# Performance work log

Measured on AMD Instinct MI355X. Metric: run time of the kernel, lower is better.

## Reference

```python
import jax, jax.numpy as jnp
import numpy as np
import math

PROJ_EPS = 0.001
C_CURV = 0.5  # hyperbolic curvature c


def setup_inputs() -> dict:
    key = jax.random.key(0)
    k1, k2, k3 = jax.random.split(key, 3)
    B, C, H, W, N = 4, 256, 256, 256, 19
    x = jax.random.normal(k1, (B, C, H, W), dtype=jnp.float32)
    # kaiming_uniform_(a=sqrt(5)) on (N, C): bound = sqrt(6 / ((1+5) * fan_in)) = 1/sqrt(C)
    bound = 1.0 / math.sqrt(C)
    P_MLR = jax.random.uniform(k2, (N, C), jnp.float32, -bound, bound)
    A_MLR = jax.random.uniform(k3, (N, C), jnp.float32, -bound, bound)
    return {"x": x, "P_MLR": P_MLR, "A_MLR": A_MLR}


def reference(x, P_MLR, A_MLR):
    K = jnp.float32(C_CURV)
    eps = jnp.float32(1e-12)

    xx = jnp.sum(x * x, axis=1)                       # (B,H,W)  ||x||^2
    pp = jnp.sum(P_MLR * P_MLR, axis=1)               # (N,)     ||-P||^2
    # 1x1 conv with kernel -P: channel contraction
    px = jnp.einsum('bchw,nc->bnhw', x, -P_MLR)       # (B,N,H,W)

    xx_b = xx[:, None]                                # (B,1,H,W)
    pp_b = pp[None, :, None, None]                    # (1,N,1,1)

    sqsq = (K * xx_b) * (K * pp_b)
    A = 1.0 + 2.0 * K * px + K * xx_b
    Bc = 1.0 - K * pp_b
    D = 1.0 + 2.0 * K * px + sqsq
    D = jnp.maximum(D, eps)
    alpha = A / D
    beta = Bc / D

    mobaddnorm = alpha * alpha * pp_b + beta * beta * xx_b + 2.0 * alpha * beta * px
    maxnorm = (1.0 - PROJ_EPS) / jnp.sqrt(K)
    sqrtm = jnp.sqrt(mobaddnorm)
    project_normalized = jnp.where(sqrtm > maxnorm,
                                   maxnorm / jnp.maximum(sqrtm, eps),
                                   jnp.ones_like(mobaddnorm))
    mobaddnormprojected = jnp.where(sqrtm < maxnorm, mobaddnorm,
                                    jnp.full_like(mobaddnorm, maxnorm * maxnorm))

    A_norm = jnp.linalg.norm(A_MLR, axis=1)           # (N,)
    normed_A = A_MLR / jnp.maximum(A_norm, eps)[:, None]  # torch F.normalize (eps=1e-12)

    xdota = beta * jnp.einsum('bchw,nc->bnhw', x, normed_A)
    pdota = alpha * jnp.sum(-P_MLR * normed_A, axis=1)[None, :, None, None]
    mobdota = (xdota + pdota) * project_normalized

    lamb_px = 2.0 / jnp.maximum(1.0 - K * mobaddnormprojected, eps)
    sineterm = jnp.sqrt(K) * mobdota * lamb_px
    out = (2.0 / jnp.sqrt(K)) * A_norm[None, :, None, None] * jnp.arcsinh(sineterm)
    return out
```

## Files before the change

### kernel.cpp

```cpp
#include <hip/hip_runtime.h>
#include <math.h>

#define C_DIM 256
#define N_DIM 19
#define HW 65536
#define CQ 64
#define PP_OFF (N_DIM * C_DIM)
#define PA_OFF (PP_OFF + 32)
#define AN_OFF (PP_OFF + 64)

__global__ void prep_kernel(const float* __restrict__ P,
                            const float* __restrict__ A,
                            float* __restrict__ ws) {
    int n = blockIdx.x;
    int lane = threadIdx.x;
    float pp = 0.f, aa = 0.f, pa = 0.f;
    for (int c = lane; c < C_DIM; c += 64) {
        float p = P[n * C_DIM + c];
        float a = A[n * C_DIM + c];
        pp += p * p;
        aa += a * a;
        pa += p * a;
    }
#pragma unroll
    for (int off = 32; off > 0; off >>= 1) {
        pp += __shfl_xor(pp, off);
        aa += __shfl_xor(aa, off);
        pa += __shfl_xor(pa, off);
    }
    float an  = sqrtf(aa);
    float inv = 1.0f / fmaxf(an, 1e-12f);
    for (int c = lane; c < C_DIM; c += 64) {
        ws[n * C_DIM + c] = A[n * C_DIM + c] * inv;
    }
    if (lane == 0) {
        ws[PP_OFF + n] = pp;
        ws[PA_OFF + n] = -pa * inv;
        ws[AN_OFF + n] = an;
    }
}

__global__ __launch_bounds__(256, 4) void hyper_mlr_main(
    const float* __restrict__ x, const float* __restrict__ P,
    const float* __restrict__ ws, float* __restrict__ out)
{
    __shared__ float4 sP4[N_DIM * CQ];
    __shared__ float4 sA4[N_DIM * CQ];
    __shared__ float  spp[N_DIM], spa[N_DIM], san[N_DIM];

    const float4* P4 = reinterpret_cast<const float4*>(P);
    const float4* W4 = reinterpret_cast<const float4*>(ws);
    for (int i = threadIdx.x; i < N_DIM * CQ; i += 256) {
        float4 pv = P4[i];
        sP4[i] = make_float4(-pv.x, -pv.y, -pv.z, -pv.w);
        sA4[i] = W4[i];
    }
    if (threadIdx.x < N_DIM) {
        spp[threadIdx.x] = ws[PP_OFF + threadIdx.x];
        spa[threadIdx.x] = ws[PA_OFF + threadIdx.x];
        san[threadIdx.x] = ws[AN_OFF + threadIdx.x];
    }
    __syncthreads();

    int tid = blockIdx.x * 256 + threadIdx.x;
    int b   = tid >> 16;
    int hw  = tid & 65535;
    const float* xb = x + (size_t)b * C_DIM * HW + hw;

    float xx = 0.f;
    float px[N_DIM], xa[N_DIM];
#pragma unroll
    for (int n = 0; n < N_DIM; ++n) { px[n] = 0.f; xa[n] = 0.f; }

    float x0 = xb[0];
    float x1 = xb[(size_t)HW];
    float x2 = xb[(size_t)2 * HW];
    float x3 = xb[(size_t)3 * HW];

#pragma unroll 2
    for (int cq = 0; cq < CQ - 1; ++cq) {
        const float* xn = xb + (size_t)(cq + 1) * 4 * HW;
        float n0 = xn[0];
        float n1 = xn[(size_t)HW];
        float n2 = xn[(size_t)2 * HW];
        float n3 = xn[(size_t)3 * HW];

        xx += x0 * x0; xx += x1 * x1; xx += x2 * x2; xx += x3 * x3;
#pragma unroll
        for (int n = 0; n < N_DIM; ++n) {
            float4 p = sP4[n * CQ + cq];
            float4 a = sA4[n * CQ + cq];
            px[n] += x0 * p.x; px[n] += x1 * p.y; px[n] += x2 * p.z; px[n] += x3 * p.w;
            xa[n] += x0 * a.x; xa[n] += x1 * a.y; xa[n] += x2 * a.z; xa[n] += x3 * a.w;
        }
        x0 = n0; x1 = n1; x2 = n2; x3 = n3;
    }
    {
        const int cq = CQ - 1;
        xx += x0 * x0; xx += x1 * x1; xx += x2 * x2; xx += x3 * x3;
#pragma unroll
        for (int n = 0; n < N_DIM; ++n) {
            float4 p = sP4[n * CQ + cq];
            float4 a = sA4[n * CQ + cq];
            px[n] += x0 * p.x; px[n] += x1 * p.y; px[n] += x2 * p.z; px[n] += x3 * p.w;
            xa[n] += x0 * a.x; xa[n] += x1 * a.y; xa[n] += x2 * a.z; xa[n] += x3 * a.w;
        }
    }

    const float K        = 0.5f;
    const float sqK      = 0.70710678118654752f;
    const float maxnorm  = 0.999f / sqK;
    const float maxnorm2 = maxnorm * maxnorm;
    const float eps      = 1e-12f;

    float* ob = out + (size_t)b * N_DIM * HW + hw;
#pragma unroll
    for (int n = 0; n < N_DIM; ++n) {
        float pp = spp[n];
        float pa = spa[n];
        float an = san[n];
        float pxs = px[n], xas = xa[n];

        float Av = 1.0f + pxs + K * xx;
        float Bv = 1.0f - K * pp;
        float D  = fmaxf(1.0f + pxs + (K * K) * xx * pp, eps);
        float alpha = Av / D, beta = Bv / D;
        float mob = alpha * alpha * pp + beta * beta * xx + 2.0f * alpha * beta * pxs;
        float sqrtm = sqrtf(fmaxf(mob, 0.0f));
        float proj = (sqrtm > maxnorm) ? (maxnorm / fmaxf(sqrtm, eps)) : 1.0f;
        float mobp = (sqrtm < maxnorm) ? mob : maxnorm2;
        float mobdota = (beta * xas + alpha * pa) * proj;
        float lamb = 2.0f / fmaxf(1.0f - K * mobp, eps);
        float sine = sqK * mobdota * lamb;
        ob[(size_t)n * HW] = (2.0f / sqK) * an * asinhf(sine);
    }
}

extern "C" void kernel_launch(void* const* d_in, const int* in_sizes, int n_in,
                              void* d_out, int out_size, void* d_ws, size_t ws_size,
                              hipStream_t stream) {
    const float* x  = (const float*)d_in[0];
    const float* P  = (const float*)d_in[1];
    const float* A  = (const float*)d_in[2];
    float* out = (float*)d_out;
    float* ws  = (float*)d_ws;

    prep_kernel<<<N_DIM, 64, 0, stream>>>(P, A, ws);
    hyper_mlr_main<<<1024, 256, 0, stream>>>(x, P, ws, out);
}
```

Measured before the change: 434.6 us.

## Read weights via uniform scalar loads from interleaved global table instead of LDS

The prep kernel now writes an interleaved table, ordered by channel-quad then class, holding negated P and normalized A. The main kernel drops its shared-memory staging and __syncthreads and reads the weights straight from global memory with wave-uniform addresses, which the compiler can turn into scalar (SMEM) loads, removing LDS traffic from the inner loop. It also drops the occupancy hint in launch_bounds and the unroll-2 pragma. The risk is scalar-cache latency and SGPR pressure in the inner loop, and possibly lower occupancy.

```diff
diff --git a/kernel.cpp b/kernel.cpp
--- a/kernel.cpp
+++ b/kernel.cpp
@@ -5,23 +5,21 @@
 #define N_DIM 19
 #define HW 65536
 #define CQ 64
-#define PP_OFF (N_DIM * C_DIM)
-#define PA_OFF (PP_OFF + 32)
-#define AN_OFF (PP_OFF + 64)
+#define TBL (CQ * N_DIM * 8)
+#define PP_OFF TBL
+#define PA_OFF (TBL + 32)
+#define AN_OFF (TBL + 64)
 
 __global__ void prep_kernel(const float* __restrict__ P,
                             const float* __restrict__ A,
                             float* __restrict__ ws) {
     int n = blockIdx.x;
     int lane = threadIdx.x;
-    float pp = 0.f, aa = 0.f, pa = 0.f;
-    for (int c = lane; c < C_DIM; c += 64) {
-        float p = P[n * C_DIM + c];
-        float a = A[n * C_DIM + c];
-        pp += p * p;
-        aa += a * a;
-        pa += p * a;
-    }
+    float4 pv = *reinterpret_cast<const float4*>(P + n * C_DIM + lane * 4);
+    float4 av = *reinterpret_cast<const float4*>(A + n * C_DIM + lane * 4);
+    float pp = pv.x * pv.x + pv.y * pv.y + pv.z * pv.z + pv.w * pv.w;
+    float aa = av.x * av.x + av.y * av.y + av.z * av.z + av.w * av.w;
+    float pa = pv.x * av.x + pv.y * av.y + pv.z * av.z + pv.w * av.w;
 #pragma unroll
     for (int off = 32; off > 0; off >>= 1) {
         pp += __shfl_xor(pp, off);
@@ -30,9 +28,11 @@
     }
     float an  = sqrtf(aa);
     float inv = 1.0f / fmaxf(an, 1e-12f);
-    for (int c = lane; c < C_DIM; c += 64) {
-        ws[n * C_DIM + c] = A[n * C_DIM + c] * inv;
-    }
+
+    float* o = ws + (size_t)(lane * N_DIM + n) * 8;
+    o[0] = -pv.x; o[1] = -pv.y; o[2] = -pv.z; o[3] = -pv.w;
+    o[4] = av.x * inv; o[5] = av.y * inv; o[6] = av.z * inv; o[7] = av.w * inv;
+
     if (lane == 0) {
         ws[PP_OFF + n] = pp;
         ws[PA_OFF + n] = -pa * inv;
@@ -40,28 +40,10 @@
     }
 }
 
-__global__ __launch_bounds__(256, 4) void hyper_mlr_main(
-    const float* __restrict__ x, const float* __restrict__ P,
-    const float* __restrict__ ws, float* __restrict__ out)
+__global__ __launch_bounds__(256) void hyper_mlr_main(
+    const float* __restrict__ x, const float* __restrict__ ws,
+    float* __restrict__ out)
 {
-    __shared__ float4 sP4[N_DIM * CQ];
-    __shared__ float4 sA4[N_DIM * CQ];
-    __shared__ float  spp[N_DIM], spa[N_DIM], san[N_DIM];
-
-    const float4* P4 = reinterpret_cast<const float4*>(P);
-    const float4* W4 = reinterpret_cast<const float4*>(ws);
-    for (int i = threadIdx.x; i < N_DIM * CQ; i += 256) {
-        float4 pv = P4[i];
-        sP4[i] = make_float4(-pv.x, -pv.y, -pv.z, -pv.w);
-        sA4[i] = W4[i];
-    }
-    if (threadIdx.x < N_DIM) {
-        spp[threadIdx.x] = ws[PP_OFF + threadIdx.x];
-        spa[threadIdx.x] = ws[PA_OFF + threadIdx.x];
-        san[threadIdx.x] = ws[AN_OFF + threadIdx.x];
-    }
-    __syncthreads();
-
     int tid = blockIdx.x * 256 + threadIdx.x;
     int b   = tid >> 16;
     int hw  = tid & 65535;
@@ -77,7 +59,6 @@
     float x2 = xb[(size_t)2 * HW];
     float x3 = xb[(size_t)3 * HW];
 
-#pragma unroll 2
     for (int cq = 0; cq < CQ - 1; ++cq) {
         const float* xn = xb + (size_t)(cq + 1) * 4 * HW;
         float n0 = xn[0];
@@ -86,10 +67,11 @@
         float n3 = xn[(size_t)3 * HW];
 
         xx += x0 * x0; xx += x1 * x1; xx += x2 * x2; xx += x3 * x3;
+        const float* wq = ws + (size_t)cq * N_DIM * 8;
 #pragma unroll
         for (int n = 0; n < N_DIM; ++n) {
-            float4 p = sP4[n * CQ + cq];
-            float4 a = sA4[n * CQ + cq];
+            float4 p = *reinterpret_cast<const float4*>(wq + n * 8);
+            float4 a = *reinterpret_cast<const float4*>(wq + n * 8 + 4);
             px[n] += x0 * p.x; px[n] += x1 * p.y; px[n] += x2 * p.z; px[n] += x3 * p.w;
             xa[n] += x0 * a.x; xa[n] += x1 * a.y; xa[n] += x2 * a.z; xa[n] += x3 * a.w;
         }
@@ -98,10 +80,11 @@
     {
         const int cq = CQ - 1;
         xx += x0 * x0; xx += x1 * x1; xx += x2 * x2; xx += x3 * x3;
+        const float* wq = ws + (size_t)cq * N_DIM * 8;
 #pragma unroll
         for (int n = 0; n < N_DIM; ++n) {
-            float4 p = sP4[n * CQ + cq];
-            float4 a = sA4[n * CQ + cq];
+            float4 p = *reinterpret_cast<const float4*>(wq + n * 8);
+            float4 a = *reinterpret_cast<const float4*>(wq + n * 8 + 4);
             px[n] += x0 * p.x; px[n] += x1 * p.y; px[n] += x2 * p.z; px[n] += x3 * p.w;
             xa[n] += x0 * a.x; xa[n] += x1 * a.y; xa[n] += x2 * a.z; xa[n] += x3 * a.w;
         }
@@ -116,9 +99,9 @@
     float* ob = out + (size_t)b * N_DIM * HW + hw;
 #pragma unroll
     for (int n = 0; n < N_DIM; ++n) {
-        float pp = spp[n];
-        float pa = spa[n];
-        float an = san[n];
+        float pp = ws[PP_OFF + n];
+        float pa = ws[PA_OFF + n];
+        float an = ws[AN_OFF + n];
         float pxs = px[n], xas = xa[n];
 
         float Av = 1.0f + pxs + K * xx;
@@ -146,5 +129,5 @@
     float* ws  = (float*)d_ws;
 
     prep_kernel<<<N_DIM, 64, 0, stream>>>(P, A, ws);
-    hyper_mlr_main<<<1024, 256, 0, stream>>>(x, P, ws, out);
+    hyper_mlr_main<<<1024, 256, 0, stream>>>(x, ws, out);
 }
```

After: 461.0 us. 6.1% more time.
